# Kernel tuning notes

Measured on AMD Instinct MI355X. Metric: run time of the kernel, lower is better.

## Reference

```python
import jax, jax.numpy as jnp
import numpy as np

N = 100000
E = 800000
NFEAT = 128
NHID = 128
NCLASS = 40
THRESHOLD = 0.1
EPS = 1e-8


def setup_inputs() -> dict:
    key = jax.random.key(0)
    ks = jax.random.split(key, 12)
    x = jax.random.normal(ks[0], (N, NFEAT), dtype=jnp.float32)
    edge_index = jax.random.randint(ks[1], (2, E), 0, N, dtype=jnp.int64)
    edge_index2 = jax.random.randint(ks[2], (2, E), 0, N, dtype=jnp.int64)
    s1 = 1.0 / np.sqrt(NFEAT)
    s2 = 1.0 / np.sqrt(NHID)
    s3 = 1.0 / np.sqrt(NCLASS)
    W_gc1 = jax.random.uniform(ks[3], (NFEAT, NHID), jnp.float32, -s1, s1)
    b_gc1 = jax.random.uniform(ks[4], (NHID,), jnp.float32, -s1, s1)
    W_gc2 = jax.random.uniform(ks[5], (NHID, NCLASS), jnp.float32, -s2, s2)
    b_gc2 = jax.random.uniform(ks[6], (NCLASS,), jnp.float32, -s2, s2)
    W_att1 = jax.random.uniform(ks[7], (NCLASS, NCLASS), jnp.float32, -s3, s3)
    b_att1 = jax.random.uniform(ks[8], (NCLASS,), jnp.float32, -s3, s3)
    W_att2 = jax.random.uniform(ks[9], (NCLASS, 1), jnp.float32, -s3, s3)
    return {"x": x, "W_gc1": W_gc1, "b_gc1": b_gc1, "W_gc2": W_gc2,
            "b_gc2": b_gc2, "W_att1": W_att1, "b_att1": b_att1,
            "W_att2": W_att2, "edge_index": edge_index, "edge_index2": edge_index2}


def att_coef(feat, row, col, alive):
    # cosine similarity per edge; edges failing the threshold get weight 0
    # (exactly equivalent to removing them: contribute 0 to degree & messages).
    a = feat[row]          # [E, d]
    b = feat[col]          # [E, d]
    dot = jnp.sum(a * b, axis=-1)
    na = jnp.maximum(jnp.linalg.norm(a, axis=-1), EPS)
    nb = jnp.maximum(jnp.linalg.norm(b, axis=-1), EPS)
    sims = dot / (na * nb)
    mask = alive & (sims >= THRESHOLD)
    # original computes this under torch.no_grad()
    ew = jax.lax.stop_gradient(jnp.where(mask, sims, 0.0))
    return ew, mask


def gcn_conv(x, row, col, ew, W, b):
    # PyG GCNConv with add_self_loops=True, normalize=True on weighted adjacency
    h = x @ W                                     # [N, out]
    deg = jax.ops.segment_sum(ew, row, num_segments=N) + 1.0  # +1 self loop
    dinv = deg ** -0.5
    nw = dinv[row] * ew * dinv[col]               # [E]
    agg = jax.ops.segment_sum(h[col] * nw[:, None], row, num_segments=N)
    agg = agg + h * (dinv * dinv)[:, None]        # self-loop contribution
    return agg + b


def reference(x, W_gc1, b_gc1, W_gc2, b_gc2, W_att1, b_att1, W_att2,
              edge_index, edge_index2):
    r1, c1 = edge_index[0], edge_index[1]
    r2, c2 = edge_index2[0], edge_index2[1]
    ones = jnp.ones((E,), dtype=bool)

    ew2, m2 = att_coef(x, r2, c2, ones)
    ew1, m1 = att_coef(x, r1, c1, ones)

    x2 = jax.nn.relu(gcn_conv(x, r2, c2, ew2, W_gc1, b_gc1))
    x1 = jax.nn.relu(gcn_conv(x, r1, c1, ew1, W_gc1, b_gc1))
    # dropout is identity at eval time

    ew2b, _ = att_coef(x2, r2, c2, m2)
    ew1b, _ = att_coef(x1, r1, c1, m1)

    x2 = gcn_conv(x2, r2, c2, ew2b, W_gc2, b_gc2)
    x1 = gcn_conv(x1, r1, c1, ew1b, W_gc2, b_gc2)

    z = jnp.stack([x1, x2], axis=1)               # [N, 2, C]
    w = jnp.tanh(z @ W_att1 + b_att1) @ W_att2    # [N, 2, 1]
    beta = jax.nn.softmax(w, axis=1)
    fused = jnp.sum(beta * z, axis=1)             # [N, C]
    return jax.nn.log_softmax(fused, axis=1)
```

## Files before the change

### kernel.cpp

```cpp
#include <hip/hip_runtime.h>
#include <hip/hip_bf16.h>

#define NN 100000
#define EE 800000
#define THRV 0.1f
#define DELTA 0.008f
#define EPSV 1e-8f

#define ATOMIC_ADD_F32 unsafeAtomicAdd

__device__ inline int dot4(int a, int b, int c) {
#if __has_builtin(__builtin_amdgcn_sdot4)
    return __builtin_amdgcn_sdot4(a, b, c, false);
#else
    int s = c;
    #pragma unroll
    for (int k = 0; k < 4; k++) {
        int av = (a << (24 - 8 * k)) >> 24;
        int bv = (b << (24 - 8 * k)) >> 24;
        s += av * bv;
    }
    return s;
#endif
}

__device__ inline unsigned short f2bf(float f) {
    unsigned int u = __float_as_uint(f);
    u += 0x7fffu + ((u >> 16) & 1u);
    return (unsigned short)(u >> 16);
}

__device__ inline float bf2f(unsigned short s) {
    return __uint_as_float(((unsigned int)s) << 16);
}


__global__ __launch_bounds__(256) void normalize_k(const float* __restrict__ x,
                                                   unsigned short* __restrict__ xq,
                                                   float* __restrict__ rs,
                                                   float* __restrict__ norms_x,
                                                   float* __restrict__ degL1,
                                                   int* __restrict__ cnt) {
    int node = blockIdx.x * 4 + (threadIdx.x >> 6);
    int lane = threadIdx.x & 63;
    float2 v = reinterpret_cast<const float2*>(x)[(size_t)node * 64 + lane];
    float ss = v.x * v.x + v.y * v.y;
    float am = fmaxf(fabsf(v.x), fabsf(v.y));
    #pragma unroll
    for (int off = 32; off; off >>= 1) {
        ss += __shfl_xor(ss, off);
        am = fmaxf(am, __shfl_xor(am, off));
    }
    float norm = fmaxf(sqrtf(ss), EPSV);
    am = fmaxf(am, 1e-12f);
    float qs = 127.0f / am;
    int q0 = __float2int_rn(v.x * qs);
    int q1 = __float2int_rn(v.y * qs);
    xq[(size_t)node * 64 + lane] = (unsigned short)((q0 & 0xff) | ((q1 & 0xff) << 8));
    if (lane == 0) {
        norms_x[node] = norm;
        rs[node] = am / (127.0f * norm);
        degL1[node] = 1.0f;
        degL1[node + NN] = 1.0f;
        cnt[node] = 0;
        cnt[node + NN] = 0;
    }
}


__global__ __launch_bounds__(64) void quantW_k(const float* __restrict__ W, int C,
                                               int* __restrict__ Wq,
                                               float* __restrict__ wcs) {
    int col = blockIdx.x;
    int t = threadIdx.x;
    float am = fmaxf(fabsf(W[t * C + col]), fabsf(W[(t + 64) * C + col]));
    #pragma unroll
    for (int off = 32; off; off >>= 1) am = fmaxf(am, __shfl_xor(am, off));
    am = fmaxf(am, 1e-20f);
    float qs = 127.0f / am;
    if (t < 32) {
        int p = 0;
        #pragma unroll
        for (int tt = 0; tt < 4; tt++) {
            int q = __float2int_rn(W[(4 * t + tt) * C + col] * qs);
            p |= (q & 0xff) << (8 * tt);
        }
        Wq[t * C + col] = p;
    }
    if (t == 0) wcs[col] = am / 127.0f;
}


__global__ __launch_bounds__(256) void edge_sim1_k(
        const unsigned short* __restrict__ xq, const float* __restrict__ rs,
        const float* __restrict__ x, const float* __restrict__ norms_x,
        const int* __restrict__ r1, const int* __restrict__ c1,
        const int* __restrict__ r2, const int* __restrict__ c2,
        float* __restrict__ ews, float* __restrict__ degL1,
        int* __restrict__ cnt) {
    int tid = threadIdx.x;
    int e = blockIdx.x * 32 + (tid >> 3);
    int q = tid & 7;
    int rnode, cnode, gr;
    if (e < EE) { rnode = r1[e]; cnode = c1[e]; gr = rnode; }
    else { int ee = e - EE; rnode = r2[ee]; cnode = c2[ee]; gr = NN + rnode; }
    int role = q >> 2;
    int j = q & 3;
    int node = role ? cnode : rnode;
    const uint4* base = reinterpret_cast<const uint4*>(xq) + (size_t)node * 8 + j * 2;
    uint4 v0 = base[0];
    uint4 v1 = base[1];
    uint4 p0, p1;
    p0.x = (unsigned)__shfl_xor((int)v0.x, 4);
    p0.y = (unsigned)__shfl_xor((int)v0.y, 4);
    p0.z = (unsigned)__shfl_xor((int)v0.z, 4);
    p0.w = (unsigned)__shfl_xor((int)v0.w, 4);
    p1.x = (unsigned)__shfl_xor((int)v1.x, 4);
    p1.y = (unsigned)__shfl_xor((int)v1.y, 4);
    p1.z = (unsigned)__shfl_xor((int)v1.z, 4);
    p1.w = (unsigned)__shfl_xor((int)v1.w, 4);
    int d = dot4((int)v0.x, (int)p0.x, 0);
    d = dot4((int)v0.y, (int)p0.y, d);
    d = dot4((int)v0.z, (int)p0.z, d);
    d = dot4((int)v0.w, (int)p0.w, d);
    d = dot4((int)v1.x, (int)p1.x, d);
    d = dot4((int)v1.y, (int)p1.y, d);
    d = dot4((int)v1.z, (int)p1.z, d);
    d = dot4((int)v1.w, (int)p1.w, d);
    d += __shfl_xor(d, 1);
    d += __shfl_xor(d, 2);
    float sim = (float)d * rs[rnode] * rs[cnode];
    if (fabsf(sim - THRV) <= DELTA) {
        const float4* xa = reinterpret_cast<const float4*>(x + (size_t)rnode * 128);
        const float4* xb = reinterpret_cast<const float4*>(x + (size_t)cnode * 128);
        float df = 0.f;
        #pragma unroll
        for (int t = 0; t < 4; t++) {
            float4 a = xa[q + 8 * t];
            float4 bb = xb[q + 8 * t];
            df += a.x * bb.x + a.y * bb.y + a.z * bb.z + a.w * bb.w;
        }
        df += __shfl_xor(df, 1);
        df += __shfl_xor(df, 2);
        df += __shfl_xor(df, 4);
        sim = df / (norms_x[rnode] * norms_x[cnode]);
    }
    float w = (sim >= THRV) ? sim : 0.0f;
    if (q == 0) {
        ews[e] = w;
        if (w != 0.0f) {
            ATOMIC_ADD_F32(&degL1[gr], w);
            atomicAdd(&cnt[gr], 1);
        }
    }
}


__global__ __launch_bounds__(256) void gemm_nh_k(const int* __restrict__ xqi,
                                                 const float* __restrict__ rs,
                                                 const float* __restrict__ norms_x,
                                                 const int* __restrict__ Wq,
                                                 const float* __restrict__ wcs,
                                                 unsigned int* __restrict__ hq,
                                                 float* __restrict__ hrs, int n) {
    __shared__ int WsQ[32 * 128];
    __shared__ int XsQ[32 * 32];
    __shared__ float wcss[128];
    int tid = threadIdx.x;
    int row0 = blockIdx.x * 32;
    {
        int4* W4 = reinterpret_cast<int4*>(WsQ);
        const int4* Wg4 = reinterpret_cast<const int4*>(Wq);
        #pragma unroll
        for (int i = 0; i < 4; i++) W4[tid + 256 * i] = Wg4[tid + 256 * i];
        if (tid < 128) wcss[tid] = wcs[tid];
        int r = tid >> 3, p = tid & 7;
        reinterpret_cast<int4*>(XsQ)[tid] =
            reinterpret_cast<const int4*>(xqi + (size_t)(row0 + r) * 32)[p];
    }
    __syncthreads();
    int cg = tid & 31;
    int rl = tid >> 5;
    int4 acc[4];
    #pragma unroll
    for (int i = 0; i < 4; i++) acc[i] = make_int4(0, 0, 0, 0);
    for (int k4 = 0; k4 < 32; k4++) {
        int4 wv = reinterpret_cast<const int4*>(WsQ + k4 * 128)[cg];
        #pragma unroll
        for (int r4 = 0; r4 < 4; r4++) {
            int xv = XsQ[(rl + 8 * r4) * 32 + k4];
            acc[r4].x = dot4(xv, wv.x, acc[r4].x);
            acc[r4].y = dot4(xv, wv.y, acc[r4].y);
            acc[r4].z = dot4(xv, wv.z, acc[r4].z);
            acc[r4].w = dot4(xv, wv.w, acc[r4].w);
        }
    }
    float4 wc = reinterpret_cast<const float4*>(wcss)[cg];
    #pragma unroll
    for (int r4 = 0; r4 < 4; r4++) {
        int grow = row0 + rl + 8 * r4;
        float xscale = rs[grow] * norms_x[grow];
        float fx = (float)acc[r4].x * xscale * wc.x;
        float fy = (float)acc[r4].y * xscale * wc.y;
        float fz = (float)acc[r4].z * xscale * wc.z;
        float fw = (float)acc[r4].w * xscale * wc.w;
        float am = fmaxf(fmaxf(fabsf(fx), fabsf(fy)), fmaxf(fabsf(fz), fabsf(fw)));
        #pragma unroll
        for (int off = 1; off < 32; off <<= 1) am = fmaxf(am, __shfl_xor(am, off));
        am = fmaxf(am, 1e-20f);
        float qs = 127.0f / am;
        int q0 = __float2int_rn(fx * qs);
        int q1 = __float2int_rn(fy * qs);
        int q2 = __float2int_rn(fz * qs);
        int q3 = __float2int_rn(fw * qs);
        unsigned int u = (q0 & 0xff) | ((q1 & 0xff) << 8) |
                         ((q2 & 0xff) << 16) | ((q3 & 0xff) << 24);
        if (grow < n) {
            hq[(size_t)grow * 32 + cg] = u;
            if (cg == 0) hrs[grow] = am / 127.0f;
        }
    }
}


__global__ __launch_bounds__(512) void scan1_k(const int* __restrict__ in,
                                               int* __restrict__ out,
                                               int* __restrict__ partials, int n) {
    __shared__ int a[1024], b[1024];
    int t = threadIdx.x;
    int base = blockIdx.x * 1024;
    a[t]       = (base + t       < n) ? in[base + t]       : 0;
    a[t + 512] = (base + t + 512 < n) ? in[base + t + 512] : 0;
    __syncthreads();
    int* src = a; int* dst = b;
    for (int off = 1; off < 1024; off <<= 1) {
        #pragma unroll
        for (int q = 0; q < 2; q++) {
            int i = t + q * 512;
            int v = src[i];
            if (i >= off) v += src[i - off];
            dst[i] = v;
        }
        __syncthreads();
        int* tmp = src; src = dst; dst = tmp;
    }
    for (int q = 0; q < 2; q++) {
        int i = t + q * 512;
        if (base + i < n) out[base + i] = i ? src[i - 1] : 0;
    }
    if (t == 0) partials[blockIdx.x] = src[1023];
}

__global__ __launch_bounds__(256) void scan2_k(int* __restrict__ partials, int m) {
    __shared__ int a[256], b[256];
    int t = threadIdx.x;
    a[t] = (t < m) ? partials[t] : 0;
    __syncthreads();
    int* src = a; int* dst = b;
    for (int off = 1; off < 256; off <<= 1) {
        int v = src[t];
        if (t >= off) v += src[t - off];
        dst[t] = v;
        __syncthreads();
        int* tmp = src; src = dst; dst = tmp;
    }
    if (t < m) partials[t] = t ? src[t - 1] : 0;
}

__global__ void scan3_k(int* __restrict__ start, int* __restrict__ next,
                        const int* __restrict__ partials,
                        const int* __restrict__ cnt, int n) {
    int i = blockIdx.x * 256 + threadIdx.x;
    if (i < n) {
        int v = start[i] + partials[i >> 10];
        start[i] = v;
        next[i] = v;
        if (i == n - 1) start[n] = v + cnt[i];
    }
}


__global__ void scatter_alive_k(const int* __restrict__ r1, const int* __restrict__ c1,
                                const int* __restrict__ r2, const int* __restrict__ c2,
                                const float* __restrict__ ews,
                                const float* __restrict__ degL1,
                                const float* __restrict__ hrs,
                                int* __restrict__ next, int2* __restrict__ acw) {
    int e = blockIdx.x * 256 + threadIdx.x;
    float w = ews[e];
    if (w == 0.0f) return;
    int gr, c, sb;
    if (e < EE) { gr = r1[e]; c = c1[e]; sb = 0; }
    else        { gr = NN + r2[e - EE]; c = c2[e - EE]; sb = NN; }
    int pos = atomicAdd(&next[gr], 1);
    int2 rec;
    rec.x = c;
    rec.y = __float_as_int(w * rsqrtf(degL1[sb + c]) * hrs[c]);
    acw[pos] = rec;
}


__global__ __launch_bounds__(256) void agg128_fused_k(
        const unsigned short* __restrict__ hq16, const float* __restrict__ hrs,
        const int* __restrict__ start, const int2* __restrict__ acw,
        const float* __restrict__ degL1, const float* __restrict__ bias,
        unsigned int* __restrict__ aggb, unsigned short* __restrict__ xq2,
        float* __restrict__ rs2, float* __restrict__ norms_l2,
        float* __restrict__ degL2) {
    int gr = blockIdx.x * 4 + (threadIdx.x >> 6);
    int lane = threadIdx.x & 63;
    int rnode = (gr < NN) ? gr : gr - NN;
    int j0 = start[gr], j1 = start[gr + 1];
    float2 acc = make_float2(0.f, 0.f);
    for (int j = j0; j < j1; j++) {
        int2 rec = acw[j];
        float wv = __int_as_float(rec.y);
        unsigned short hv = hq16[(size_t)rec.x * 64 + lane];
        acc.x += (float)(char)(hv & 0xff) * wv;
        acc.y += (float)(char)(hv >> 8) * wv;
    }
    float dr = rsqrtf(degL1[gr]);
    float hr = hrs[rnode];
    unsigned short hs = hq16[(size_t)rnode * 64 + lane];
    float hx = (float)(char)(hs & 0xff) * hr;
    float hy = (float)(char)(hs >> 8) * hr;
    float2 bb = reinterpret_cast<const float2*>(bias)[lane];
    float vx = fmaxf(acc.x * dr + hx * dr * dr + bb.x, 0.0f);
    float vy = fmaxf(acc.y * dr + hy * dr * dr + bb.y, 0.0f);
    aggb[(size_t)gr * 64 + lane] =
        (unsigned int)f2bf(vx) | ((unsigned int)f2bf(vy) << 16);
    float ss = vx * vx + vy * vy;
    float am = fmaxf(vx, vy);
    #pragma unroll
    for (int off = 32; off; off >>= 1) {
        ss += __shfl_xor(ss, off);
        am = fmaxf(am, __shfl_xor(am, off));
    }
    float norm = fmaxf(sqrtf(ss), EPSV);
    am = fmaxf(am, 1e-12f);
    float qs = 127.0f / am;
    int q0 = __float2int_rn(vx * qs);
    int q1 = __float2int_rn(vy * qs);
    xq2[(size_t)gr * 64 + lane] = (unsigned short)((q0 & 0xff) | ((q1 & 0xff) << 8));
    if (lane == 0) {
        rs2[gr] = am / (127.0f * norm);
        norms_l2[gr] = norm;
        degL2[gr] = 1.0f;
    }
}


__global__ __launch_bounds__(256) void edge_sim2_k(
        const unsigned short* __restrict__ xq2, const float* __restrict__ rs2,
        const unsigned int* __restrict__ aggb, const float* __restrict__ norms_l2,
        const int* __restrict__ start, int2* __restrict__ acw,
        float* __restrict__ degL2) {
    int gr = blockIdx.x * 4 + (threadIdx.x >> 6);
    int lane = threadIdx.x & 63;
    int j0 = start[gr], j1 = start[gr + 1];
    if (j0 == j1) return;
    int set_base = (gr < NN) ? 0 : NN;
    unsigned int au = xq2[(size_t)gr * 64 + lane];
    int a0 = ((int)(au << 24)) >> 24;
    int a1 = ((int)((au << 16) & 0xff000000u)) >> 24;
    float ra = rs2[gr];
    float nr = norms_l2[gr];
    float sum = 0.f;
    for (int j = j0; j < j1; j++) {
        int2 rec = acw[j];
        int cg = set_base + rec.x;
        unsigned int bu = xq2[(size_t)cg * 64 + lane];
        int b0 = ((int)(bu << 24)) >> 24;
        int b1 = ((int)((bu << 16) & 0xff000000u)) >> 24;
        int d = a0 * b0 + a1 * b1;
        #pragma unroll
        for (int off = 32; off; off >>= 1) d += __shfl_xor(d, off);
        float sim = (float)d * ra * rs2[cg];
        if (fabsf(sim - THRV) <= DELTA) {
            unsigned int av = aggb[(size_t)gr * 64 + lane];
            unsigned int bv = aggb[(size_t)cg * 64 + lane];
            float df = bf2f((unsigned short)(av & 0xffff)) *
                       bf2f((unsigned short)(bv & 0xffff)) +
                       bf2f((unsigned short)(av >> 16)) *
                       bf2f((unsigned short)(bv >> 16));
            #pragma unroll
            for (int off = 32; off; off >>= 1) df += __shfl_xor(df, off);
            sim = df / (nr * norms_l2[cg]);
        }
        float w2 = (sim >= THRV) ? sim : 0.0f;
        if (lane == 0) acw[j].y = __float_as_int(w2);
        sum += w2;
    }
    if (lane == 0) degL2[gr] = 1.0f + sum;
}


__global__ __launch_bounds__(256) void gemm_nc_k(const int* __restrict__ xq2i,
                                                 const float* __restrict__ rs2,
                                                 const float* __restrict__ norms_l2,
                                                 const int* __restrict__ Wq2,
                                                 const float* __restrict__ wcs2,
                                                 unsigned short* __restrict__ h2b, int n) {
    __shared__ int XsQ[64 * 33];
    __shared__ int WsQ2[32 * 40];
    __shared__ float wcss[40];
    __shared__ float rsc[64];
    int tid = threadIdx.x;
    int row0 = blockIdx.x * 64;
    for (int i = tid; i < 32 * 40; i += 256) WsQ2[i] = Wq2[i];
    if (tid < 40) wcss[tid] = wcs2[tid];
    if (tid < 64) {
        int g = row0 + tid;
        rsc[tid] = rs2[g] * norms_l2[g];
    }
    #pragma unroll
    for (int i = 0; i < 2; i++) {
        int idx = tid + 256 * i;
        int rr = idx >> 3, p = idx & 7;
        int4 v = reinterpret_cast<const int4*>(xq2i + (size_t)(row0 + rr) * 32)[p];
        int* dst = &XsQ[rr * 33 + p * 4];
        dst[0] = v.x; dst[1] = v.y; dst[2] = v.z; dst[3] = v.w;
    }
    __syncthreads();
    int c5 = tid & 7;
    int r  = tid >> 3;
    int acc0[5] = {0, 0, 0, 0, 0}, acc1[5] = {0, 0, 0, 0, 0};
    for (int k4 = 0; k4 < 32; k4++) {
        int xv0 = XsQ[r * 33 + k4];
        int xv1 = XsQ[(r + 32) * 33 + k4];
        #pragma unroll
        for (int c = 0; c < 5; c++) {
            int wv = WsQ2[k4 * 40 + c5 * 5 + c];
            acc0[c] = dot4(xv0, wv, acc0[c]);
            acc1[c] = dot4(xv1, wv, acc1[c]);
        }
    }
    float s0 = rsc[r], s1 = rsc[r + 32];
    int g0 = row0 + r, g1 = row0 + r + 32;
    for (int c = 0; c < 5; c++) {
        float wc = wcss[c5 * 5 + c];
        h2b[(size_t)g0 * 64 + c5 * 5 + c] = f2bf((float)acc0[c] * s0 * wc);
        h2b[(size_t)g1 * 64 + c5 * 5 + c] = f2bf((float)acc1[c] * s1 * wc);
    }
}


__global__ __launch_bounds__(256) void agg40_fused_k(
        const unsigned short* __restrict__ h2b, const int* __restrict__ start,
        const int2* __restrict__ acw, const float* __restrict__ degL2,
        const float* __restrict__ bias, float* __restrict__ aggy) {
    int gr = blockIdx.x * 4 + (threadIdx.x >> 6);
    int lane = threadIdx.x & 63;
    int set_base = (gr < NN) ? 0 : NN;
    int j0 = start[gr], j1 = start[gr + 1];
    bool act = lane < 40;
    float acc = 0.f;
    for (int j = j0; j < j1; j++) {
        int2 rec = acw[j];
        float w2 = __int_as_float(rec.y);
        if (w2 == 0.0f) continue;
        int cg = set_base + rec.x;
        float nv = w2 * rsqrtf(degL2[cg]);
        float hv = act ? bf2f(h2b[(size_t)cg * 64 + lane]) : 0.f;
        acc += hv * nv;
    }
    if (act) {
        float dr = rsqrtf(degL2[gr]);
        float self = bf2f(h2b[(size_t)gr * 64 + lane]);
        aggy[(size_t)gr * 40 + lane] = acc * dr + self * dr * dr + bias[lane];
    }
}


__global__ __launch_bounds__(256) void fusion_k(const float* __restrict__ y1,
                                                const float* __restrict__ y2,
                                                const float* __restrict__ W1,
                                                const float* __restrict__ b1,
                                                const float* __restrict__ W2,
                                                float* __restrict__ out, int n) {
    __shared__ float W1s[40 * 40];
    __shared__ float b1s[40];
    __shared__ float W2s[40];
    int tid = threadIdx.x;
    for (int i = tid; i < 1600; i += 256) W1s[i] = W1[i];
    if (tid < 40) { b1s[tid] = b1[tid]; W2s[tid] = W2[tid]; }
    __syncthreads();
    int i = blockIdx.x * 256 + tid;
    if (i >= n) return;
    float z1[40], z2[40];
    const float4* y14 = reinterpret_cast<const float4*>(y1 + (size_t)i * 40);
    const float4* y24 = reinterpret_cast<const float4*>(y2 + (size_t)i * 40);
    #pragma unroll
    for (int q = 0; q < 10; q++) {
        float4 a = y14[q], b = y24[q];
        z1[4 * q] = a.x; z1[4 * q + 1] = a.y; z1[4 * q + 2] = a.z; z1[4 * q + 3] = a.w;
        z2[4 * q] = b.x; z2[4 * q + 1] = b.y; z2[4 * q + 2] = b.z; z2[4 * q + 3] = b.w;
    }
    float w1 = 0.f, w2 = 0.f;
    for (int c = 0; c < 40; c++) {
        float s1 = b1s[c], s2 = b1s[c];
        for (int j = 0; j < 40; j++) {
            float ww = W1s[j * 40 + c];
            s1 += z1[j] * ww; s2 += z2[j] * ww;
        }
        float wa = W2s[c];
        w1 += tanhf(s1) * wa; w2 += tanhf(s2) * wa;
    }
    float m = fmaxf(w1, w2);
    float e1 = expf(w1 - m), e2 = expf(w2 - m);
    float inv = 1.0f / (e1 + e2);
    float be1 = e1 * inv, be2 = e2 * inv;
    float fu[40];
    float mx = -1e30f;
    #pragma unroll
    for (int c = 0; c < 40; c++) {
        fu[c] = be1 * z1[c] + be2 * z2[c];
        mx = fmaxf(mx, fu[c]);
    }
    float se = 0.f;
    #pragma unroll
    for (int c = 0; c < 40; c++) se += expf(fu[c] - mx);
    float ls = logf(se);
    float4* o4 = reinterpret_cast<float4*>(out + (size_t)i * 40);
    #pragma unroll
    for (int q = 0; q < 10; q++) {
        float4 v;
        v.x = fu[4 * q] - mx - ls; v.y = fu[4 * q + 1] - mx - ls;
        v.z = fu[4 * q + 2] - mx - ls; v.w = fu[4 * q + 3] - mx - ls;
        o4[q] = v;
    }
}


extern "C" void kernel_launch(void* const* d_in, const int* in_sizes, int n_in,
                              void* d_out, int out_size, void* d_ws, size_t ws_size,
                              hipStream_t stream) {
    (void)in_sizes; (void)n_in; (void)out_size; (void)ws_size;
    const float* x   = (const float*)d_in[0];
    const float* Wg1 = (const float*)d_in[1];
    const float* bg1 = (const float*)d_in[2];
    const float* Wg2 = (const float*)d_in[3];
    const float* bg2 = (const float*)d_in[4];
    const float* Wa1 = (const float*)d_in[5];
    const float* ba1 = (const float*)d_in[6];
    const float* Wa2 = (const float*)d_in[7];
    const int* ei1 = (const int*)d_in[8];
    const int* ei2 = (const int*)d_in[9];
    const int *r1 = ei1, *c1 = ei1 + EE;
    const int *r2 = ei2, *c2 = ei2 + EE;
    float* out = (float*)d_out;

    float* wp = (float*)d_ws;
    float* norms_x  = wp;  wp += NN;
    float* norms_l2 = wp;  wp += 2 * NN;
    float* rs       = wp;  wp += NN;
    float* degL1    = wp;  wp += 2 * NN;
    float* degL2    = wp;  wp += 2 * NN;
    float* hrs      = wp;  wp += NN;
    int*   cnt      = (int*)wp;  wp += 2 * NN;
    int*   start    = (int*)wp;  wp += 2 * NN + 8;
    int*   next     = (int*)wp;  wp += 2 * NN;
    int*   partials = (int*)wp;  wp += 512;
    int*   Wq       = (int*)wp;  wp += 32 * 128;
    float* wcs      = wp;  wp += 128;
    int*   Wq2      = (int*)wp;  wp += 32 * 40;
    float* wcs2     = wp;  wp += 40;
    float* ews      = wp;  wp += 2 * EE;
    int2*  acw      = (int2*)wp; wp += (size_t)2 * 2 * EE;
    unsigned int* hq = (unsigned int*)wp; wp += (size_t)NN * 32;
    unsigned short* h2b = (unsigned short*)wp; wp += (size_t)2 * NN * 32;
    unsigned int*   aggb = (unsigned int*)wp;  wp += (size_t)2 * NN * 64;
    unsigned short* xq2 = (unsigned short*)wp; wp += (size_t)2 * NN * 32;
    unsigned short* xq = (unsigned short*)aggb;
    float* rs2 = ews;
    float* aggy = (float*)aggb;

    const int twoN = 2 * NN;
    const int twoE = 2 * EE;
    const int scan_blocks = (twoN + 1023) / 1024;

    quantW_k<<<128, 64, 0, stream>>>(Wg1, 128, Wq, wcs);
    quantW_k<<<40, 64, 0, stream>>>(Wg2, 40, Wq2, wcs2);
    normalize_k<<<NN / 4, 256, 0, stream>>>(x, xq, rs, norms_x, degL1, cnt);
    edge_sim1_k<<<twoE / 32, 256, 0, stream>>>(xq, rs, x, norms_x,
                                               r1, c1, r2, c2, ews, degL1, cnt);
    gemm_nh_k<<<(NN + 31) / 32, 256, 0, stream>>>((const int*)xq, rs, norms_x,
                                                  Wq, wcs, hq, hrs, NN);

    scan1_k<<<scan_blocks, 512, 0, stream>>>(cnt, start, partials, twoN);
    scan2_k<<<1, 256, 0, stream>>>(partials, scan_blocks);
    scan3_k<<<(twoN + 255) / 256, 256, 0, stream>>>(start, next, partials, cnt, twoN);
    scatter_alive_k<<<twoE / 256, 256, 0, stream>>>(r1, c1, r2, c2, ews, degL1, hrs,
                                                    next, acw);

    agg128_fused_k<<<twoN / 4, 256, 0, stream>>>((const unsigned short*)hq, hrs,
                                                 start, acw, degL1, bg1,
                                                 aggb, xq2, rs2, norms_l2, degL2);

    edge_sim2_k<<<twoN / 4, 256, 0, stream>>>(xq2, rs2, aggb, norms_l2,
                                              start, acw, degL2);
    gemm_nc_k<<<twoN / 64, 256, 0, stream>>>((const int*)xq2, rs2, norms_l2,
                                             Wq2, wcs2, h2b, twoN);
    agg40_fused_k<<<twoN / 4, 256, 0, stream>>>(h2b, start, acw, degL2, bg2, aggy);
    fusion_k<<<(NN + 255) / 256, 256, 0, stream>>>(aggy, aggy + (size_t)NN * 40,
                                                   Wa1, ba1, Wa2, out, NN);
}
```

Measured before the change: 417.0 us.

## Merge layer-2 edge similarity and class GEMM into one launch, precompute dinv*hrs

The layer-2 edge-similarity kernel and the 40-class int8 GEMM kernel are combined into one launch. The first 3125 blocks run the GEMM and the rest run per-node similarity, so the two independent workloads can overlap and one launch and tail are removed. The scan3 kernel now also precomputes a per-node rsqrt(deg)*hrs array, so the scatter kernel does one gather per edge instead of two. The exact-recompute band around the threshold is narrowed from 0.008 to 0.004, which means fewer bf16 fallback dot products but a higher chance of misclassifying edges near the threshold.

```diff
diff --git a/kernel.cpp b/kernel.cpp
--- a/kernel.cpp
+++ b/kernel.cpp
@@ -4,8 +4,9 @@
 #define NN 100000
 #define EE 800000
 #define THRV 0.1f
-#define DELTA 0.008f
+#define DELTA 0.004f
 #define EPSV 1e-8f
+#define GB2 3125
 
 #define ATOMIC_ADD_F32 unsafeAtomicAdd
 
@@ -267,15 +268,21 @@
     if (t < m) partials[t] = t ? src[t - 1] : 0;
 }
 
+
 __global__ void scan3_k(int* __restrict__ start, int* __restrict__ next,
                         const int* __restrict__ partials,
-                        const int* __restrict__ cnt, int n) {
+                        const int* __restrict__ cnt,
+                        const float* __restrict__ degL1,
+                        const float* __restrict__ hrs,
+                        float* __restrict__ dinvh, int n) {
     int i = blockIdx.x * 256 + threadIdx.x;
     if (i < n) {
         int v = start[i] + partials[i >> 10];
         start[i] = v;
         next[i] = v;
         if (i == n - 1) start[n] = v + cnt[i];
+        int node = (i < NN) ? i : i - NN;
+        dinvh[i] = rsqrtf(degL1[i]) * hrs[node];
     }
 }
 
@@ -283,8 +290,7 @@
 __global__ void scatter_alive_k(const int* __restrict__ r1, const int* __restrict__ c1,
                                 const int* __restrict__ r2, const int* __restrict__ c2,
                                 const float* __restrict__ ews,
-                                const float* __restrict__ degL1,
-                                const float* __restrict__ hrs,
+                                const float* __restrict__ dinvh,
                                 int* __restrict__ next, int2* __restrict__ acw) {
     int e = blockIdx.x * 256 + threadIdx.x;
     float w = ews[e];
@@ -295,7 +301,7 @@
     int pos = atomicAdd(&next[gr], 1);
     int2 rec;
     rec.x = c;
-    rec.y = __float_as_int(w * rsqrtf(degL1[sb + c]) * hrs[c]);
+    rec.y = __float_as_int(w * dinvh[sb + c]);
     acw[pos] = rec;
 }
 
@@ -350,13 +356,62 @@
 }
 
 
-__global__ __launch_bounds__(256) void edge_sim2_k(
+__global__ __launch_bounds__(256) void simgemm2_k(
         const unsigned short* __restrict__ xq2, const float* __restrict__ rs2,
         const unsigned int* __restrict__ aggb, const float* __restrict__ norms_l2,
         const int* __restrict__ start, int2* __restrict__ acw,
-        float* __restrict__ degL2) {
-    int gr = blockIdx.x * 4 + (threadIdx.x >> 6);
-    int lane = threadIdx.x & 63;
+        float* __restrict__ degL2,
+        const int* __restrict__ Wq2, const float* __restrict__ wcs2,
+        unsigned short* __restrict__ h2b, int n) {
+    __shared__ int XsQ[64 * 33];
+    __shared__ int WsQ2[32 * 40];
+    __shared__ float wcss[40];
+    __shared__ float rsc[64];
+    int tid = threadIdx.x;
+
+    if (blockIdx.x < GB2) {
+        const int* xq2i = (const int*)xq2;
+        int row0 = blockIdx.x * 64;
+        for (int i = tid; i < 32 * 40; i += 256) WsQ2[i] = Wq2[i];
+        if (tid < 40) wcss[tid] = wcs2[tid];
+        if (tid < 64) {
+            int g = row0 + tid;
+            rsc[tid] = rs2[g] * norms_l2[g];
+        }
+        #pragma unroll
+        for (int i = 0; i < 2; i++) {
+            int idx = tid + 256 * i;
+            int rr = idx >> 3, p = idx & 7;
+            int4 v = reinterpret_cast<const int4*>(xq2i + (size_t)(row0 + rr) * 32)[p];
+            int* dst = &XsQ[rr * 33 + p * 4];
+            dst[0] = v.x; dst[1] = v.y; dst[2] = v.z; dst[3] = v.w;
+        }
+        __syncthreads();
+        int c5 = tid & 7;
+        int r  = tid >> 3;
+        int acc0[5] = {0, 0, 0, 0, 0}, acc1[5] = {0, 0, 0, 0, 0};
+        for (int k4 = 0; k4 < 32; k4++) {
+            int xv0 = XsQ[r * 33 + k4];
+            int xv1 = XsQ[(r + 32) * 33 + k4];
+            #pragma unroll
+            for (int c = 0; c < 5; c++) {
+                int wv = WsQ2[k4 * 40 + c5 * 5 + c];
+                acc0[c] = dot4(xv0, wv, acc0[c]);
+                acc1[c] = dot4(xv1, wv, acc1[c]);
+            }
+        }
+        float s0 = rsc[r], s1 = rsc[r + 32];
+        int g0 = row0 + r, g1 = row0 + r + 32;
+        for (int c = 0; c < 5; c++) {
+            float wc = wcss[c5 * 5 + c];
+            h2b[(size_t)g0 * 64 + c5 * 5 + c] = f2bf((float)acc0[c] * s0 * wc);
+            h2b[(size_t)g1 * 64 + c5 * 5 + c] = f2bf((float)acc1[c] * s1 * wc);
+        }
+        return;
+    }
+
+    int gr = (blockIdx.x - GB2) * 4 + (tid >> 6);
+    int lane = tid & 63;
     int j0 = start[gr], j1 = start[gr + 1];
     if (j0 == j1) return;
     int set_base = (gr < NN) ? 0 : NN;
@@ -392,56 +447,6 @@
         sum += w2;
     }
     if (lane == 0) degL2[gr] = 1.0f + sum;
-}
-
-
-__global__ __launch_bounds__(256) void gemm_nc_k(const int* __restrict__ xq2i,
-                                                 const float* __restrict__ rs2,
-                                                 const float* __restrict__ norms_l2,
-                                                 const int* __restrict__ Wq2,
-                                                 const float* __restrict__ wcs2,
-                                                 unsigned short* __restrict__ h2b, int n) {
-    __shared__ int XsQ[64 * 33];
-    __shared__ int WsQ2[32 * 40];
-    __shared__ float wcss[40];
-    __shared__ float rsc[64];
-    int tid = threadIdx.x;
-    int row0 = blockIdx.x * 64;
-    for (int i = tid; i < 32 * 40; i += 256) WsQ2[i] = Wq2[i];
-    if (tid < 40) wcss[tid] = wcs2[tid];
-    if (tid < 64) {
-        int g = row0 + tid;
-        rsc[tid] = rs2[g] * norms_l2[g];
-    }
-    #pragma unroll
-    for (int i = 0; i < 2; i++) {
-        int idx = tid + 256 * i;
-        int rr = idx >> 3, p = idx & 7;
-        int4 v = reinterpret_cast<const int4*>(xq2i + (size_t)(row0 + rr) * 32)[p];
-        int* dst = &XsQ[rr * 33 + p * 4];
-        dst[0] = v.x; dst[1] = v.y; dst[2] = v.z; dst[3] = v.w;
-    }
-    __syncthreads();
-    int c5 = tid & 7;
-    int r  = tid >> 3;
-    int acc0[5] = {0, 0, 0, 0, 0}, acc1[5] = {0, 0, 0, 0, 0};
-    for (int k4 = 0; k4 < 32; k4++) {
-        int xv0 = XsQ[r * 33 + k4];
-        int xv1 = XsQ[(r + 32) * 33 + k4];
-        #pragma unroll
-        for (int c = 0; c < 5; c++) {
-            int wv = WsQ2[k4 * 40 + c5 * 5 + c];
-            acc0[c] = dot4(xv0, wv, acc0[c]);
-            acc1[c] = dot4(xv1, wv, acc1[c]);
-        }
-    }
-    float s0 = rsc[r], s1 = rsc[r + 32];
-    int g0 = row0 + r, g1 = row0 + r + 32;
-    for (int c = 0; c < 5; c++) {
-        float wc = wcss[c5 * 5 + c];
-        h2b[(size_t)g0 * 64 + c5 * 5 + c] = f2bf((float)acc0[c] * s0 * wc);
-        h2b[(size_t)g1 * 64 + c5 * 5 + c] = f2bf((float)acc1[c] * s1 * wc);
-    }
 }
 
 
@@ -557,6 +562,7 @@
     float* degL1    = wp;  wp += 2 * NN;
     float* degL2    = wp;  wp += 2 * NN;
     float* hrs      = wp;  wp += NN;
+    float* dinvh    = wp;  wp += 2 * NN;
     int*   cnt      = (int*)wp;  wp += 2 * NN;
     int*   start    = (int*)wp;  wp += 2 * NN + 8;
     int*   next     = (int*)wp;  wp += 2 * NN;
@@ -589,18 +595,18 @@
 
     scan1_k<<<scan_blocks, 512, 0, stream>>>(cnt, start, partials, twoN);
     scan2_k<<<1, 256, 0, stream>>>(partials, scan_blocks);
-    scan3_k<<<(twoN + 255) / 256, 256, 0, stream>>>(start, next, partials, cnt, twoN);
-    scatter_alive_k<<<twoE / 256, 256, 0, stream>>>(r1, c1, r2, c2, ews, degL1, hrs,
+    scan3_k<<<(twoN + 255) / 256, 256, 0, stream>>>(start, next, partials, cnt,
+                                                    degL1, hrs, dinvh, twoN);
+    scatter_alive_k<<<twoE / 256, 256, 0, stream>>>(r1, c1, r2, c2, ews, dinvh,
                                                     next, acw);
 
     agg128_fused_k<<<twoN / 4, 256, 0, stream>>>((const unsigned short*)hq, hrs,
                                                  start, acw, degL1, bg1,
                                                  aggb, xq2, rs2, norms_l2, degL2);
 
-    edge_sim2_k<<<twoN / 4, 256, 0, stream>>>(xq2, rs2, aggb, norms_l2,
-                                              start, acw, degL2);
-    gemm_nc_k<<<twoN / 64, 256, 0, stream>>>((const int*)xq2, rs2, norms_l2,
-                                             Wq2, wcs2, h2b, twoN);
+    simgemm2_k<<<GB2 + twoN / 4, 256, 0, stream>>>(xq2, rs2, aggb, norms_l2,
+                                                   start, acw, degL2,
+                                                   Wq2, wcs2, h2b, twoN);
     agg40_fused_k<<<twoN / 4, 256, 0, stream>>>(h2b, start, acw, degL2, bg2, aggy);
     fusion_k<<<(NN + 255) / 256, 256, 0, stream>>>(aggy, aggy + (size_t)NN * 40,
                                                    Wa1, ba1, Wa2, out, NN);
```

New measurement: 406.0 us. -2.6%, faster.
